# Optimization experiments

Measured on AMD Instinct MI355X. Metric: run time of the kernel, lower is better.

The kernel has to match this reference:

```python
import jax, jax.numpy as jnp
import numpy as np

WS = 7          # window size
NH = 12         # attention heads
D_STATE = 64    # mamba d_state
HEADDIM = 64    # mamba headdim


def layernorm(x, w, b):
    mu = jnp.mean(x, axis=-1, keepdims=True)
    var = jnp.mean((x - mu) ** 2, axis=-1, keepdims=True)
    return (x - mu) * jax.lax.rsqrt(var + 1e-5) * w + b


def mamba2(x, W_in, conv_w, conv_b, dt_bias, A_log, D, mnorm_w, W_out):
    # Mamba2 (SSD) forward: in_proj -> causal depthwise conv+silu -> selective scan -> gated RMSNorm -> out_proj
    B, L, dm = x.shape
    nheads = dt_bias.shape[0]
    d_inner = nheads * HEADDIM
    zxbcdt = x @ W_in                                   # (B,L,2*d_inner+2*d_state+nheads)
    z = zxbcdt[..., :d_inner]
    xBC = zxbcdt[..., d_inner:2 * d_inner + 2 * D_STATE]
    dt = zxbcdt[..., -nheads:]
    conv_dim = xBC.shape[-1]
    pad = conv_w.shape[-1] - 1
    xBC_t = jnp.swapaxes(xBC, 1, 2)                     # (B, conv_dim, L)
    conv_out = jax.lax.conv_general_dilated(
        xBC_t, conv_w[:, None, :], window_strides=(1,), padding=[(pad, 0)],
        feature_group_count=conv_dim, dimension_numbers=('NCH', 'OIH', 'NCH'))
    xBC = jax.nn.silu(jnp.swapaxes(conv_out, 1, 2) + conv_b)
    xs = xBC[..., :d_inner]
    Bm = xBC[..., d_inner:d_inner + D_STATE]            # (B,L,n)
    Cm = xBC[..., d_inner + D_STATE:]                   # (B,L,n)
    dt = jax.nn.softplus(dt + dt_bias)                  # (B,L,h)
    A = -jnp.exp(A_log)                                 # (h,)
    dA = jnp.exp(dt * A)                                # (B,L,h)
    xh = xs.reshape(B, L, nheads, HEADDIM)              # (B,L,h,p)

    def step(h, inp):
        dA_t, dt_t, x_t, B_t, C_t = inp                 # (B,h),(B,h),(B,h,p),(B,n),(B,n)
        dBx = (dt_t[..., None] * x_t)[..., None] * B_t[:, None, None, :]
        h = h * dA_t[..., None, None] + dBx             # (B,h,p,n)
        y = jnp.einsum('bhpn,bn->bhp', h, C_t)
        return h, y

    sw = lambda a: jnp.swapaxes(a, 0, 1)                # time-major
    h0 = jnp.zeros((B, nheads, HEADDIM, D_STATE), x.dtype)
    _, ys = jax.lax.scan(step, h0, (sw(dA), sw(dt), sw(xh), sw(Bm), sw(Cm)))
    y = jnp.swapaxes(ys, 0, 1) + D[None, None, :, None] * xh   # (B,L,h,p)
    y = y.reshape(B, L, d_inner)
    g = y * jax.nn.silu(z)                              # gated RMSNorm (norm_before_gate=False)
    g = g * jax.lax.rsqrt(jnp.mean(g * g, axis=-1, keepdims=True) + 1e-5) * mnorm_w
    return g @ W_out


def gated_window_attention(xw, qkv_w, qkv_b, gate_w, gate_b, proj_w, proj_b):
    B_, N, C = xw.shape
    hd = C // NH
    qkv = (xw @ qkv_w + qkv_b).reshape(B_, N, 3, NH, hd).transpose(2, 0, 3, 1, 4)
    q, k, v = qkv[0] * (hd ** -0.5), qkv[1], qkv[2]     # (B_,h,N,d)
    attn = jax.nn.softmax(jnp.einsum('bhnd,bhmd->bhnm', q, k), axis=-1)
    xa = jnp.einsum('bhnm,bhmd->bhnd', attn, v).transpose(0, 2, 1, 3)  # (B_,N,h,d)
    gate = jax.nn.sigmoid(xw @ gate_w + gate_b)[..., None]             # (B_,N,h,1)
    xa = (xa * gate).reshape(B_, N, C)
    return xa @ proj_w + proj_b


def lgs_forward(x, norm1_w, norm1_b, W_in, conv_w, conv_b, dt_bias, A_log, D, mnorm_w, W_out,
                qkv_w, qkv_b, gate_w, gate_b, proj_w, proj_b, fusion_w, fusion_b,
                norm2_w, norm2_b, fc1_w, fc1_b, fc2_w, fc2_b, H, W):
    B, L, C = x.shape
    shortcut = x
    xn = layernorm(x, norm1_w, norm1_b)
    # Branch A: Mamba2 global scan
    x_mamba = mamba2(xn, W_in, conv_w, conv_b, dt_bias, A_log, D, mnorm_w, W_out)
    # Branch B: gated window attention (shift_size=0 -> no roll, no mask)
    x2d = xn.reshape(B, H, W, C)
    xw = x2d.reshape(B, H // WS, WS, W // WS, WS, C).transpose(0, 1, 3, 2, 4, 5).reshape(-1, WS * WS, C)
    aw = gated_window_attention(xw, qkv_w, qkv_b, gate_w, gate_b, proj_w, proj_b)
    x_attn = aw.reshape(B, H // WS, W // WS, WS, WS, C).transpose(0, 1, 3, 2, 4, 5).reshape(B, L, C)
    # Fuse branches with 1x1 conv (== linear on channel dim)
    x_cat = jnp.concatenate([x_mamba, x_attn], axis=-1)   # (B,L,2C)
    x_fused = x_cat @ fusion_w + fusion_b
    x = shortcut + x_fused
    xn2 = layernorm(x, norm2_w, norm2_b)
    mlp = jax.nn.gelu(xn2 @ fc1_w + fc1_b, approximate=False) @ fc2_w + fc2_b
    return x + mlp


def setup_inputs() -> dict:
    key = jax.random.key(0)
    ks = jax.random.split(key, 16)
    B, H, W, C = 8, 56, 56, 384
    L = H * W
    d_inner, d_state, nheads_m, d_conv = 768, 64, 12, 4
    d_in_proj = 2 * d_inner + 2 * d_state + nheads_m   # 1676
    conv_dim = d_inner + 2 * d_state                   # 896
    s = 0.02
    return {
        'x': jax.random.normal(ks[0], (B, L, C), jnp.float32),
        'norm1_w': jnp.ones((C,), jnp.float32),
        'norm1_b': jnp.zeros((C,), jnp.float32),
        'W_in': jax.random.normal(ks[1], (C, d_in_proj), jnp.float32) * s,
        'conv_w': jax.random.normal(ks[2], (conv_dim, d_conv), jnp.float32) * 0.1,
        'conv_b': jnp.zeros((conv_dim,), jnp.float32),
        'dt_bias': jax.random.normal(ks[3], (nheads_m,), jnp.float32) * 0.5,
        'A_log': jnp.log(jax.random.uniform(ks[4], (nheads_m,), jnp.float32, 1.0, 16.0)),
        'D': jnp.ones((nheads_m,), jnp.float32),
        'mnorm_w': jnp.ones((d_inner,), jnp.float32),
        'W_out': jax.random.normal(ks[5], (d_inner, C), jnp.float32) * s,
        'qkv_w': jax.random.normal(ks[6], (C, 3 * C), jnp.float32) * s,
        'qkv_b': jnp.zeros((3 * C,), jnp.float32),
        'gate_w': jax.random.normal(ks[7], (C, NH), jnp.float32) * s,
        'gate_b': jnp.zeros((NH,), jnp.float32),
        'proj_w': jax.random.normal(ks[8], (C, C), jnp.float32) * s,
        'proj_b': jnp.zeros((C,), jnp.float32),
        'fusion_w': jax.random.normal(ks[9], (2 * C, C), jnp.float32) * s,
        'fusion_b': jnp.zeros((C,), jnp.float32),
        'norm2_w': jnp.ones((C,), jnp.float32),
        'norm2_b': jnp.zeros((C,), jnp.float32),
        'fc1_w': jax.random.normal(ks[10], (C, 4 * C), jnp.float32) * s,
        'fc1_b': jnp.zeros((4 * C,), jnp.float32),
        'fc2_w': jax.random.normal(ks[11], (4 * C, C), jnp.float32) * s,
        'fc2_b': jnp.zeros((C,), jnp.float32),
        'H': H,
        'W': W,
    }


def reference(x, norm1_w, norm1_b, W_in, conv_w, conv_b, dt_bias, A_log, D, mnorm_w, W_out,
              qkv_w, qkv_b, gate_w, gate_b, proj_w, proj_b, fusion_w, fusion_b,
              norm2_w, norm2_b, fc1_w, fc1_b, fc2_w, fc2_b, H, W):
    return lgs_forward(x, norm1_w, norm1_b, W_in, conv_w, conv_b, dt_bias, A_log, D, mnorm_w, W_out,
                       qkv_w, qkv_b, gate_w, gate_b, proj_w, proj_b, fusion_w, fusion_b,
                       norm2_w, norm2_b, fc1_w, fc1_b, fc2_w, fc2_b, H, W)
```

## Files before the change

kernel.cpp:

```cpp
#include <hip/hip_runtime.h>
#include <math.h>

static constexpr int L_SEQ  = 3136;
static constexpr int NBATCH = 8;
static constexpr int CDIM   = 384;
static constexpr int DIN    = 768;
static constexpr int NHM    = 12;
static constexpr int HDM    = 64;
static constexpr int DPROJ  = 1676;
static constexpr int CONVD  = 896;
static constexpr int NROWS  = NBATCH * L_SEQ;
static constexpr int NHA    = 12;
static constexpr int NCH    = 49;
static constexpr int CHT    = 64;
static constexpr int CTK    = 28;
static constexpr int ZXLD   = 1024;

typedef __attribute__((ext_vector_type(8))) short short8;
typedef __attribute__((ext_vector_type(8))) unsigned short ushort8;
typedef __attribute__((ext_vector_type(4))) float f32x4;
typedef const unsigned int __attribute__((address_space(1)))* gua_t;
typedef unsigned int __attribute__((address_space(3)))* lua_t;

__device__ __forceinline__ float siluf(float x) { return x / (1.f + __expf(-x)); }
__device__ __forceinline__ unsigned short f2bf(float f) {
  unsigned int u = __float_as_uint(f);
  u += 0x7fff + ((u >> 16) & 1);
  return (unsigned short)(u >> 16);
}
__device__ __forceinline__ float bf2f(unsigned short h) {
  return __uint_as_float(((unsigned int)h) << 16);
}
__device__ __forceinline__ float fast_erff(float x) {
  float ax = fabsf(x);
  float tt = 1.f / (1.f + 0.3275911f * ax);
  float y = tt * (0.254829592f + tt * (-0.284496736f + tt * (1.421413741f +
            tt * (-1.453152027f + tt * 1.061405429f))));
  float r = 1.f - y * __expf(-ax * ax);
  return copysignf(r, x);
}

__global__ __launch_bounds__(256) void ln_kernel(const float* __restrict__ in,
    const float* __restrict__ w, const float* __restrict__ b, unsigned short* __restrict__ out) {
  int wave = threadIdx.x >> 6, lane = threadIdx.x & 63;
  int row = blockIdx.x * 4 + wave;
  if (row >= NROWS) return;
  const float* r = in + (size_t)row * CDIM;
  float2 v[3];
  float s1 = 0.f, s2 = 0.f;
#pragma unroll
  for (int q = 0; q < 3; q++) {
    v[q] = *(const float2*)&r[q * 128 + lane * 2];
    s1 += v[q].x + v[q].y;
    s2 += v[q].x * v[q].x + v[q].y * v[q].y;
  }
#pragma unroll
  for (int o = 32; o > 0; o >>= 1) { s1 += __shfl_xor(s1, o, 64); s2 += __shfl_xor(s2, o, 64); }
  float mu = s1 * (1.f / 384.f);
  float var = s2 * (1.f / 384.f) - mu * mu;
  float rs = rsqrtf(var + 1e-5f);
  unsigned short* o = out + (size_t)row * CDIM;
#pragma unroll
  for (int q = 0; q < 3; q++) {
    int c = q * 128 + lane * 2;
    float2 wv = *(const float2*)&w[c];
    float2 bv = *(const float2*)&b[c];
    float ox = (v[q].x - mu) * rs * wv.x + bv.x;
    float oy = (v[q].y - mu) * rs * wv.y + bv.y;
    unsigned int pk = (unsigned int)f2bf(ox) | ((unsigned int)f2bf(oy) << 16);
    *(unsigned int*)&o[c] = pk;
  }
}

__global__ __launch_bounds__(256) void wconv_kernel(const float* __restrict__ W,
    unsigned short* __restrict__ WT, int K, int N, int ldw) {
  __shared__ float tile[32][33];
  int k0 = blockIdx.x * 32, n0 = blockIdx.y * 32;
  int tx = threadIdx.x & 31, ty = threadIdx.x >> 5;
#pragma unroll
  for (int j = 0; j < 4; j++) {
    int k = k0 + ty + j * 8;
    int n = n0 + tx;
    tile[ty + j * 8][tx] = (n < N) ? W[(size_t)k * ldw + n] : 0.f;
  }
  __syncthreads();
#pragma unroll
  for (int j = 0; j < 4; j++) {
    int n = n0 + ty + j * 8;
    int k = k0 + tx;
    WT[(size_t)n * K + k] = f2bf(tile[tx][ty + j * 8]);
  }
}

template<int ACT, bool HASBIAS, bool HASRES, bool OUTBF>
__global__ __launch_bounds__(256, 4) void gemm_bf(
    const unsigned short* __restrict__ A, const unsigned short* __restrict__ WT,
    void* __restrict__ Cp, const float* __restrict__ bias,
    const float* __restrict__ res, int ldr,
    int M, int N, int K, int lda, int ldc, int coff)
{
  __shared__ unsigned short SMEM[16384];
  int t = threadIdx.x;
  int gx = gridDim.x;
  int nwg = gx * gridDim.y;
  int orig = blockIdx.y * gx + blockIdx.x;
  int qq = nwg >> 3, rr = nwg & 7;
  int xcd = orig & 7, seq = orig >> 3;
  int wgid = (xcd < rr ? xcd * (qq + 1) : rr * (qq + 1) + (xcd - rr) * qq) + seq;
  int m0 = (wgid / gx) * 128, n0 = (wgid % gx) * 128;

  int lane = t & 63, w = t >> 6;
  int wr = (w >> 1) * 64, wc = (w & 1) * 64;
  int fl = lane & 15, kq = lane >> 4;
  int so = (kq ^ ((lane >> 1) & 3)) * 8;

  int srow = t >> 2, sq = t & 3;
  int q0 = sq ^ ((srow >> 1) & 3);
  const unsigned short* pA0 = A  + (size_t)(m0 + srow) * lda + q0 * 8;
  const unsigned short* pA1 = A  + (size_t)(m0 + 64 + srow) * lda + q0 * 8;
  const unsigned short* pW0 = WT + (size_t)(n0 + srow) * K + q0 * 8;
  const unsigned short* pW1 = WT + (size_t)(n0 + 64 + srow) * K + q0 * 8;

  f32x4 acc[4][4];
#pragma unroll
  for (int i = 0; i < 4; i++)
#pragma unroll
    for (int j = 0; j < 4; j++) acc[i][j] = (f32x4)0.f;

  auto STAGE = [&](int buf) {
    unsigned short* as = SMEM + buf * 4096;
    unsigned short* ws = SMEM + 8192 + buf * 4096;
    __builtin_amdgcn_global_load_lds((gua_t)pA0, (lua_t)as + t * 4, 16, 0, 0);
    __builtin_amdgcn_global_load_lds((gua_t)pA1, (lua_t)(as + 2048) + t * 4, 16, 0, 0);
    __builtin_amdgcn_global_load_lds((gua_t)pW0, (lua_t)ws + t * 4, 16, 0, 0);
    __builtin_amdgcn_global_load_lds((gua_t)pW1, (lua_t)(ws + 2048) + t * 4, 16, 0, 0);
    pA0 += 32; pA1 += 32; pW0 += 32; pW1 += 32;
  };

  int nk = K >> 5;
  STAGE(0);
  asm volatile("s_waitcnt vmcnt(0)" ::: "memory");
  __builtin_amdgcn_s_barrier();
  asm volatile("" ::: "memory");
  __builtin_amdgcn_sched_barrier(0);
  int buf = 0;
  for (int ks = 0; ks < nk; ks++) {
    if (ks + 1 < nk) STAGE(buf ^ 1);
    const unsigned short* as = SMEM + buf * 4096;
    const unsigned short* ws = SMEM + 8192 + buf * 4096;
    short8 af[4], bfr[4];
#pragma unroll
    for (int mi = 0; mi < 4; mi++) af[mi] = *(const short8*)&as[(wr + mi * 16 + fl) * 32 + so];
#pragma unroll
    for (int ni = 0; ni < 4; ni++) bfr[ni] = *(const short8*)&ws[(wc + ni * 16 + fl) * 32 + so];
#pragma unroll
    for (int mi = 0; mi < 4; mi++)
#pragma unroll
      for (int ni = 0; ni < 4; ni++)
        acc[mi][ni] = __builtin_amdgcn_mfma_f32_16x16x32_bf16(af[mi], bfr[ni], acc[mi][ni], 0, 0, 0);
    if (ks + 1 < nk) {
      asm volatile("s_waitcnt vmcnt(0)" ::: "memory");
      __builtin_amdgcn_s_barrier();
      asm volatile("" ::: "memory");
      __builtin_amdgcn_sched_barrier(0);
      buf ^= 1;
    }
  }
  int rbase = kq * 4, cl = fl;
  if (OUTBF) {
    __builtin_amdgcn_s_barrier();
#pragma unroll
    for (int mi = 0; mi < 4; mi++)
#pragma unroll
      for (int ni = 0; ni < 4; ni++) {
        int n = wc + ni * 16 + cl;
        float bv = HASBIAS ? bias[n0 + n] : 0.f;
#pragma unroll
        for (int r = 0; r < 4; r++) {
          float v = acc[mi][ni][r] + bv;
          if (ACT == 1) v = 0.5f * v * (1.f + fast_erff(v * 0.70710678118654752f));
          SMEM[(wr + mi * 16 + rbase + r) * 128 + n] = f2bf(v);
        }
      }
    __builtin_amdgcn_s_barrier();
    unsigned short* outp = (unsigned short*)Cp + coff + n0;
#pragma unroll
    for (int it2 = 0; it2 < 8; it2++) {
      int c = it2 * 256 + t;
      int rrow = c >> 4, c8 = (c & 15) * 8;
      ushort8 v8 = *(const ushort8*)&SMEM[rrow * 128 + c8];
      *(ushort8*)&outp[(size_t)(m0 + rrow) * ldc + c8] = v8;
    }
  } else {
#pragma unroll
    for (int mi = 0; mi < 4; mi++) {
#pragma unroll
      for (int ni = 0; ni < 4; ni++) {
        int n = n0 + wc + ni * 16 + cl;
        if (n >= N) continue;
#pragma unroll
        for (int r = 0; r < 4; r++) {
          int m = m0 + wr + mi * 16 + rbase + r;
          float v = acc[mi][ni][r];
          if (HASBIAS) v += bias[n];
          if (ACT == 1) v = 0.5f * v * (1.f + fast_erff(v * 0.70710678118654752f));
          if (HASRES) v += res[(size_t)m * ldr + n];
          ((float*)Cp)[(size_t)m * ldc + coff + n] = v;
        }
      }
    }
  }
}

__global__ void dtprep_kernel(const unsigned short* __restrict__ ZX, const float* __restrict__ dt_bias,
    const float* __restrict__ A_log, float* __restrict__ DT, float* __restrict__ DA) {
  int idx = blockIdx.x * blockDim.x + threadIdx.x;
  if (idx >= NROWS * NHM) return;
  int h = idx % NHM;
  int row = idx / NHM;
  float v = bf2f(ZX[(size_t)row * ZXLD + 896 + h]) + dt_bias[h];
  float sp = (v > 20.f) ? v : log1pf(expf(v));
  DT[idx] = sp;
  DA[idx] = -expf(A_log[h]) * sp;
}

__global__ __launch_bounds__(256) void conv_bf_kernel(const unsigned short* __restrict__ xbc,
    const float* __restrict__ cw, const float* __restrict__ cb, unsigned short* __restrict__ XC,
    int ldin) {
  int t = blockIdx.x * 256 + threadIdx.x;
  int c8 = t % 112;
  int rg = t / 112;
  int b = rg / 112, lc = rg % 112;
  int l0 = lc * CTK;
  int c0 = c8 * 8;
  float w0[8], w1[8], w2[8], w3[8], bq[8];
#pragma unroll
  for (int i = 0; i < 8; i++) {
    bq[i] = cb[c0 + i];
    float4 w4 = *(const float4*)&cw[(c0 + i) * 4];
    w0[i] = w4.x; w1[i] = w4.y; w2[i] = w4.z; w3[i] = w4.w;
  }
  const unsigned short* base = xbc + (size_t)b * L_SEQ * ldin + c0;
  unsigned short* obase = XC + (size_t)b * L_SEQ * CONVD + c0;
  ushort8 h0 = (ushort8)0, h1 = (ushort8)0, h2 = (ushort8)0;
  if (l0 >= 3) {
    h0 = *(const ushort8*)&base[(size_t)(l0 - 3) * ldin];
    h1 = *(const ushort8*)&base[(size_t)(l0 - 2) * ldin];
    h2 = *(const ushort8*)&base[(size_t)(l0 - 1) * ldin];
  }
  for (int i = 0; i < CTK; i++) {
    ushort8 cur = *(const ushort8*)&base[(size_t)(l0 + i) * ldin];
    ushort8 ov;
#pragma unroll
    for (int q = 0; q < 8; q++) {
      float acc = bq[q] + w0[q] * bf2f(h0[q]) + w1[q] * bf2f(h1[q])
                + w2[q] * bf2f(h2[q]) + w3[q] * bf2f(cur[q]);
      ov[q] = f2bf(siluf(acc));
    }
    *(ushort8*)&obase[(size_t)(l0 + i) * CONVD] = ov;
    h0 = h1; h1 = h2; h2 = cur;
  }
}

__global__ __launch_bounds__(256) void mscan1_kernel(const unsigned short* __restrict__ XC,
    const float* __restrict__ dtp, const float* __restrict__ dta,
    float* __restrict__ H, float* __restrict__ QS) {
  __shared__ unsigned short Xt[64 * 72];
  __shared__ unsigned short Bt[64 * 72];
  __shared__ float lcs[64];
  __shared__ float wss[64];
  int ch = blockIdx.x, bh = blockIdx.y;
  int b = bh / NHM, head = bh - b * NHM;
  int t = threadIdx.x;
  int l0 = ch * CHT;
  const unsigned short* xcb = XC + ((size_t)b * L_SEQ + l0) * CONVD;
  if (t < 64) {
    size_t ro = ((size_t)b * L_SEQ + l0 + t) * NHM + head;
    float s = dta[ro];
#pragma unroll
    for (int o = 1; o < 64; o <<= 1) {
      float u = __shfl_up(s, o, 64);
      if (t >= o) s += u;
    }
    float lc63 = __shfl(s, 63, 64);
    lcs[t] = s;
    wss[t] = dtp[ro] * __expf(lc63 - s);
    if (t == 63) QS[bh * NCH + ch] = __expf(s);
  }
  __syncthreads();
#pragma unroll
  for (int it = 0; it < 16; it++) {
    int e = it * 256 + t;
    int j = e >> 6, cc = e & 63;
    const unsigned short* rowp = xcb + (size_t)j * CONVD;
    Xt[cc * 72 + j] = rowp[head * HDM + cc];
    Bt[cc * 72 + j] = f2bf(bf2f(rowp[768 + cc]) * wss[j]);
  }
  __syncthreads();
  int lane = t & 63, w = t >> 6;
  int wr = (w >> 1) * 32, wc = (w & 1) * 32;
  int fl = lane & 15, kq = lane >> 4;
  f32x4 acc[2][2];
#pragma unroll
  for (int i = 0; i < 2; i++)
#pragma unroll
    for (int j = 0; j < 2; j++) acc[i][j] = (f32x4)0.f;
#pragma unroll
  for (int kk = 0; kk < 2; kk++) {
    short8 af[2], bfr[2];
#pragma unroll
    for (int mi = 0; mi < 2; mi++)
      af[mi] = *(const short8*)&Xt[(wr + mi * 16 + fl) * 72 + kk * 32 + kq * 8];
#pragma unroll
    for (int ni = 0; ni < 2; ni++)
      bfr[ni] = *(const short8*)&Bt[(wc + ni * 16 + fl) * 72 + kk * 32 + kq * 8];
#pragma unroll
    for (int mi = 0; mi < 2; mi++)
#pragma unroll
      for (int ni = 0; ni < 2; ni++)
        acc[mi][ni] = __builtin_amdgcn_mfma_f32_16x16x32_bf16(af[mi], bfr[ni], acc[mi][ni], 0, 0, 0);
  }
  float* Hp = H + ((size_t)bh * NCH + ch) * 4096;
  int rbase = kq * 4, cl = fl;
#pragma unroll
  for (int mi = 0; mi < 2; mi++)
#pragma unroll
    for (int ni = 0; ni < 2; ni++)
#pragma unroll
      for (int r = 0; r < 4; r++)
        Hp[(size_t)(wr + mi * 16 + rbase + r) * 64 + wc + ni * 16 + cl] = acc[mi][ni][r];
}

__global__ __launch_bounds__(64) void scomb_kernel(float* __restrict__ H,
    const float* __restrict__ QS) {
  int bh = blockIdx.x;
  int e = (blockIdx.y * 64 + threadIdx.x) * 4;
  float4 cur = make_float4(0.f, 0.f, 0.f, 0.f);
  for (int s = 0; s < NCH; s++) {
    float* Hp = H + ((size_t)bh * NCH + s) * 4096 + e;
    float q = QS[bh * NCH + s];
    float4 tmp = *(float4*)Hp;
    *(float4*)Hp = cur;
    cur.x = q * cur.x + tmp.x;
    cur.y = q * cur.y + tmp.y;
    cur.z = q * cur.z + tmp.z;
    cur.w = q * cur.w + tmp.w;
  }
}

__global__ __launch_bounds__(256) void mscan2_kernel(const unsigned short* __restrict__ XC,
    const float* __restrict__ dtp, const float* __restrict__ dta,
    const float* __restrict__ H, const float* __restrict__ Dp,
    unsigned short* __restrict__ Ybf) {
  __shared__ unsigned short Cs[64 * 72];
  __shared__ unsigned short Bs[64 * 72];
  __shared__ unsigned short Xt[64 * 72];
  __shared__ unsigned short Hs[64 * 72];
  __shared__ unsigned short Ss[64 * 72];
  __shared__ float lcs[64];
  __shared__ float dts[64];
  int ch = blockIdx.x, bh = blockIdx.y;
  int b = bh / NHM, head = bh - b * NHM;
  int t = threadIdx.x;
  int l0 = ch * CHT;
  const unsigned short* xcb = XC + ((size_t)b * L_SEQ + l0) * CONVD;
  const float* Hg = H + ((size_t)bh * NCH + ch) * 4096;
  if (t < 64) {
    size_t ro = ((size_t)b * L_SEQ + l0 + t) * NHM + head;
    float s = dta[ro];
#pragma unroll
    for (int o = 1; o < 64; o <<= 1) {
      float u = __shfl_up(s, o, 64);
      if (t >= o) s += u;
    }
    lcs[t] = s;
    dts[t] = dtp[ro];
  }
#pragma unroll
  for (int it = 0; it < 16; it++) {
    int e = it * 256 + t;
    int j = e >> 6, cc = e & 63;
    const unsigned short* rowp = xcb + (size_t)j * CONVD;
    Xt[cc * 72 + j] = rowp[head * HDM + cc];
    Bs[j * 72 + cc] = rowp[768 + cc];
    Cs[j * 72 + cc] = rowp[832 + cc];
    Hs[j * 72 + cc] = f2bf(Hg[e]);
  }
  __syncthreads();
  int lane = t & 63, w = t >> 6;
  int wr = (w >> 1) * 32, wc = (w & 1) * 32;
  int fl = lane & 15, kq = lane >> 4;
  int rbase = kq * 4, cl = fl;
  f32x4 sacc[2][2];
#pragma unroll
  for (int i = 0; i < 2; i++)
#pragma unroll
    for (int j = 0; j < 2; j++) sacc[i][j] = (f32x4)0.f;
#pragma unroll
  for (int kk = 0; kk < 2; kk++) {
    short8 af[2], bfr[2];
#pragma unroll
    for (int mi = 0; mi < 2; mi++)
      af[mi] = *(const short8*)&Cs[(wr + mi * 16 + fl) * 72 + kk * 32 + kq * 8];
#pragma unroll
    for (int ni = 0; ni < 2; ni++)
      bfr[ni] = *(const short8*)&Bs[(wc + ni * 16 + fl) * 72 + kk * 32 + kq * 8];
#pragma unroll
    for (int mi = 0; mi < 2; mi++)
#pragma unroll
      for (int ni = 0; ni < 2; ni++)
        sacc[mi][ni] = __builtin_amdgcn_mfma_f32_16x16x32_bf16(af[mi], bfr[ni], sacc[mi][ni], 0, 0, 0);
  }
  __syncthreads();
#pragma unroll
  for (int mi = 0; mi < 2; mi++)
#pragma unroll
    for (int ni = 0; ni < 2; ni++)
#pragma unroll
      for (int r = 0; r < 4; r++) {
        int i = wr + mi * 16 + rbase + r;
        int j = wc + ni * 16 + cl;
        float v = (j <= i) ? sacc[mi][ni][r] * dts[j] * __expf(lcs[i] - lcs[j]) : 0.f;
        Ss[i * 72 + j] = f2bf(v);
      }
#pragma unroll
  for (int it = 0; it < 16; it++) {
    int e = it * 256 + t;
    int i = e >> 6, n = e & 63;
    float cv = bf2f(Cs[i * 72 + n]) * __expf(lcs[i]);
    Cs[i * 72 + n] = f2bf(cv);
  }
  __syncthreads();
  f32x4 yacc[2][2];
#pragma unroll
  for (int i = 0; i < 2; i++)
#pragma unroll
    for (int j = 0; j < 2; j++) yacc[i][j] = (f32x4)0.f;
#pragma unroll
  for (int kk = 0; kk < 2; kk++) {
    short8 af[2], bfr[2];
#pragma unroll
    for (int mi = 0; mi < 2; mi++)
      af[mi] = *(const short8*)&Ss[(wr + mi * 16 + fl) * 72 + kk * 32 + kq * 8];
#pragma unroll
    for (int ni = 0; ni < 2; ni++)
      bfr[ni] = *(const short8*)&Xt[(wc + ni * 16 + fl) * 72 + kk * 32 + kq * 8];
#pragma unroll
    for (int mi = 0; mi < 2; mi++)
#pragma unroll
      for (int ni = 0; ni < 2; ni++)
        yacc[mi][ni] = __builtin_amdgcn_mfma_f32_16x16x32_bf16(af[mi], bfr[ni], yacc[mi][ni], 0, 0, 0);
  }
#pragma unroll
  for (int kk = 0; kk < 2; kk++) {
    short8 af[2], bfr[2];
#pragma unroll
    for (int mi = 0; mi < 2; mi++)
      af[mi] = *(const short8*)&Cs[(wr + mi * 16 + fl) * 72 + kk * 32 + kq * 8];
#pragma unroll
    for (int ni = 0; ni < 2; ni++)
      bfr[ni] = *(const short8*)&Hs[(wc + ni * 16 + fl) * 72 + kk * 32 + kq * 8];
#pragma unroll
    for (int mi = 0; mi < 2; mi++)
#pragma unroll
      for (int ni = 0; ni < 2; ni++)
        yacc[mi][ni] = __builtin_amdgcn_mfma_f32_16x16x32_bf16(af[mi], bfr[ni], yacc[mi][ni], 0, 0, 0);
  }
  float Dh = Dp[head];
  unsigned short* yb = Ybf + ((size_t)b * L_SEQ + l0) * DIN + head * HDM;
#pragma unroll
  for (int mi = 0; mi < 2; mi++)
#pragma unroll
    for (int ni = 0; ni < 2; ni++)
#pragma unroll
      for (int r = 0; r < 4; r++) {
        int i = wr + mi * 16 + rbase + r;
        int p = wc + ni * 16 + cl;
        float xval = bf2f(Xt[p * 72 + i]);
        yb[(size_t)i * DIN + p] = f2bf(yacc[mi][ni][r] + Dh * xval);
      }
}

__global__ __launch_bounds__(256) void gate_rms_kernel(unsigned short* __restrict__ Y,
    const unsigned short* __restrict__ Z, const float* __restrict__ mw) {
  int wave = threadIdx.x >> 6, lane = threadIdx.x & 63;
  int row = blockIdx.x * 4 + wave;
  if (row >= NROWS) return;
  unsigned short* y = Y + (size_t)row * DIN;
  const unsigned short* z = Z + (size_t)row * DIN;
  float g[12];
  float ss = 0.f;
#pragma unroll
  for (int q = 0; q < 3; q++) {
    int c = q * 256 + lane * 4;
    uint2 yu = *(const uint2*)&y[c];
    uint2 zu = *(const uint2*)&z[c];
    float y0 = bf2f((unsigned short)(yu.x & 0xffff));
    float y1 = bf2f((unsigned short)(yu.x >> 16));
    float y2 = bf2f((unsigned short)(yu.y & 0xffff));
    float y3 = bf2f((unsigned short)(yu.y >> 16));
    float z0 = bf2f((unsigned short)(zu.x & 0xffff));
    float z1 = bf2f((unsigned short)(zu.x >> 16));
    float z2 = bf2f((unsigned short)(zu.y & 0xffff));
    float z3 = bf2f((unsigned short)(zu.y >> 16));
    float g0 = y0 * siluf(z0), g1 = y1 * siluf(z1);
    float g2 = y2 * siluf(z2), g3 = y3 * siluf(z3);
    ss += g0 * g0 + g1 * g1 + g2 * g2 + g3 * g3;
    g[q * 4 + 0] = g0; g[q * 4 + 1] = g1; g[q * 4 + 2] = g2; g[q * 4 + 3] = g3;
  }
#pragma unroll
  for (int o = 32; o > 0; o >>= 1) ss += __shfl_xor(ss, o, 64);
  float rs = rsqrtf(ss * (1.f / 768.f) + 1e-5f);
#pragma unroll
  for (int q = 0; q < 3; q++) {
    int c = q * 256 + lane * 4;
    float4 m = *(const float4*)&mw[c];
    unsigned int lo = (unsigned int)f2bf(g[q*4+0] * rs * m.x) | ((unsigned int)f2bf(g[q*4+1] * rs * m.y) << 16);
    unsigned int hi = (unsigned int)f2bf(g[q*4+2] * rs * m.z) | ((unsigned int)f2bf(g[q*4+3] * rs * m.w) << 16);
    uint2 pk; pk.x = lo; pk.y = hi;
    *(uint2*)&y[c] = pk;
  }
}

__global__ __launch_bounds__(256) void attgate_kernel(const unsigned short* __restrict__ XN,
    const float* __restrict__ gw, const float* __restrict__ gb, float* __restrict__ G) {
  int wave = threadIdx.x >> 6, lane = threadIdx.x & 63;
  int row = blockIdx.x * 4 + wave;
  if (row >= NROWS) return;
  const unsigned short* x = XN + (size_t)row * CDIM;
  float acc[12] = {};
#pragma unroll
  for (int q = 0; q < 6; q++) {
    int k = q * 64 + lane;
    float xv = bf2f(x[k]);
    const float* wr = gw + (size_t)k * 12;
    float4 w0 = *(const float4*)&wr[0];
    float4 w1 = *(const float4*)&wr[4];
    float4 w2 = *(const float4*)&wr[8];
    acc[0] += xv * w0.x; acc[1] += xv * w0.y; acc[2]  += xv * w0.z; acc[3]  += xv * w0.w;
    acc[4] += xv * w1.x; acc[5] += xv * w1.y; acc[6]  += xv * w1.z; acc[7]  += xv * w1.w;
    acc[8] += xv * w2.x; acc[9] += xv * w2.y; acc[10] += xv * w2.z; acc[11] += xv * w2.w;
  }
#pragma unroll
  for (int h = 0; h < 12; h++)
#pragma unroll
    for (int o = 32; o > 0; o >>= 1) acc[h] += __shfl_xor(acc[h], o, 64);
  if (lane == 0) {
#pragma unroll
    for (int h = 0; h < 12; h++) {
      float v = acc[h] + gb[h];
      G[(size_t)row * 12 + h] = 1.f / (1.f + expf(-v));
    }
  }
}

__global__ __launch_bounds__(64) void attn_kernel(const unsigned short* __restrict__ QKV,
    const float* __restrict__ G, unsigned short* __restrict__ XA) {
  __shared__ unsigned short Pl[64 * 72];
  __shared__ unsigned short Vt[32 * 72];
  int blk = blockIdx.x;
  int head = blk % NHA;
  int win = blk / NHA;
  int b = win >> 6;
  int wrw = win & 63;
  int wy = wrw >> 3, wx = wrw & 7;
  int lane = threadIdx.x;
  int fl = lane & 15, kq = lane >> 4;
  const float scale = 0.17677669529663688f;
  size_t bbase = (size_t)b * L_SEQ;
  const unsigned short* qb = QKV + head * 32;

  short8 aq[4], bk[4];
#pragma unroll
  for (int ti = 0; ti < 4; ti++) {
    int tok = ti * 16 + fl; if (tok > 48) tok = 48;
    int iy = tok / 7, ix = tok - iy * 7;
    size_t r = bbase + (size_t)(wy * 7 + iy) * 56 + wx * 7 + ix;
    aq[ti] = *(const short8*)&qb[r * 1152 + kq * 8];
    bk[ti] = *(const short8*)&qb[r * 1152 + 384 + kq * 8];
  }
#pragma unroll
  for (int it = 0; it < 4; it++) {
    int j = (lane >> 2) + it * 16;
    int dc = (lane & 3) * 8;
    ushort8 v8 = (ushort8)0;
    if (j <= 48) {
      int iy = j / 7, ix = j - iy * 7;
      size_t r = bbase + (size_t)(wy * 7 + iy) * 56 + wx * 7 + ix;
      v8 = *(const ushort8*)&qb[r * 1152 + 768 + dc];
    }
#pragma unroll
    for (int q2 = 0; q2 < 8; q2++) {
      int d = dc + q2;
      Vt[d * 72 + (((j >> 3) ^ (d >> 3)) << 3) + (j & 7)] = v8[q2];
    }
  }
  f32x4 sacc[4][4];
#pragma unroll
  for (int tj = 0; tj < 4; tj++)
#pragma unroll
    for (int ti = 0; ti < 4; ti++)
      sacc[tj][ti] = __builtin_amdgcn_mfma_f32_16x16x32_bf16(bk[tj], aq[ti], (f32x4)0.f, 0, 0, 0);
#pragma unroll
  for (int ti = 0; ti < 4; ti++) {
    float mx = -1e30f;
#pragma unroll
    for (int tj = 0; tj < 4; tj++)
#pragma unroll
      for (int r = 0; r < 4; r++) {
        int j = tj * 16 + kq * 4 + r;
        float v = (j < 49) ? sacc[tj][ti][r] * scale : -1e30f;
        sacc[tj][ti][r] = v;
        mx = fmaxf(mx, v);
      }
    mx = fmaxf(mx, __shfl_xor(mx, 16, 64));
    mx = fmaxf(mx, __shfl_xor(mx, 32, 64));
    float sum = 0.f;
#pragma unroll
    for (int tj = 0; tj < 4; tj++)
#pragma unroll
      for (int r = 0; r < 4; r++) {
        float e = __expf(sacc[tj][ti][r] - mx);
        sacc[tj][ti][r] = e;
        sum += e;
      }
    sum += __shfl_xor(sum, 16, 64);
    sum += __shfl_xor(sum, 32, 64);
    float inv = 1.f / sum;
    int i = ti * 16 + fl;
#pragma unroll
    for (int tj = 0; tj < 4; tj++)
#pragma unroll
      for (int r = 0; r < 4; r++) {
        int j = tj * 16 + kq * 4 + r;
        Pl[i * 72 + j] = f2bf(sacc[tj][ti][r] * inv);
      }
  }
  f32x4 oacc[4][2];
#pragma unroll
  for (int i2 = 0; i2 < 4; i2++)
#pragma unroll
    for (int nd = 0; nd < 2; nd++) oacc[i2][nd] = (f32x4)0.f;
#pragma unroll
  for (int kk = 0; kk < 2; kk++) {
    short8 ap[4], bv[2];
#pragma unroll
    for (int i2 = 0; i2 < 4; i2++)
      ap[i2] = *(const short8*)&Pl[(i2 * 16 + fl) * 72 + kk * 32 + kq * 8];
#pragma unroll
    for (int nd = 0; nd < 2; nd++) {
      int d = nd * 16 + fl;
      bv[nd] = *(const short8*)&Vt[d * 72 + (((kk * 4 + kq) ^ (d >> 3)) << 3)];
    }
#pragma unroll
    for (int i2 = 0; i2 < 4; i2++)
#pragma unroll
      for (int nd = 0; nd < 2; nd++)
        oacc[i2][nd] = __builtin_amdgcn_mfma_f32_16x16x32_bf16(ap[i2], bv[nd], oacc[i2][nd], 0, 0, 0);
  }
#pragma unroll
  for (int i2 = 0; i2 < 4; i2++) {
#pragma unroll
    for (int r = 0; r < 4; r++) {
      int i = i2 * 16 + kq * 4 + r;
      if (i > 48) continue;
      int iy = i / 7, ix = i - iy * 7;
      size_t rg = bbase + (size_t)(wy * 7 + iy) * 56 + wx * 7 + ix;
      float g = G[rg * 12 + head];
#pragma unroll
      for (int nd = 0; nd < 2; nd++)
        XA[rg * CDIM + head * 32 + nd * 16 + fl] = f2bf(oacc[i2][nd][r] * g);
    }
  }
}

extern "C" void kernel_launch(void* const* d_in, const int* in_sizes, int n_in,
                              void* d_out, int out_size, void* d_ws, size_t ws_size,
                              hipStream_t stream) {
  const float* x        = (const float*)d_in[0];
  const float* norm1_w  = (const float*)d_in[1];
  const float* norm1_b  = (const float*)d_in[2];
  const float* W_in     = (const float*)d_in[3];
  const float* conv_w   = (const float*)d_in[4];
  const float* conv_b   = (const float*)d_in[5];
  const float* dt_bias  = (const float*)d_in[6];
  const float* A_log    = (const float*)d_in[7];
  const float* Dp       = (const float*)d_in[8];
  const float* mnorm_w  = (const float*)d_in[9];
  const float* W_out    = (const float*)d_in[10];
  const float* qkv_w    = (const float*)d_in[11];
  const float* qkv_b    = (const float*)d_in[12];
  const float* gate_w   = (const float*)d_in[13];
  const float* gate_b   = (const float*)d_in[14];
  const float* proj_w   = (const float*)d_in[15];
  const float* proj_b   = (const float*)d_in[16];
  const float* fusion_w = (const float*)d_in[17];
  const float* fusion_b = (const float*)d_in[18];
  const float* norm2_w  = (const float*)d_in[19];
  const float* norm2_b  = (const float*)d_in[20];
  const float* fc1_w    = (const float*)d_in[21];
  const float* fc1_b    = (const float*)d_in[22];
  const float* fc2_w    = (const float*)d_in[23];
  const float* fc2_b    = (const float*)d_in[24];
  float* OUT = (float*)d_out;

  float* ws = (float*)d_ws;
  unsigned short* XNBF = (unsigned short*)ws;
  float* XC_  = ws + 4816896;
  float* SCR  = XC_ + 22478848;
  unsigned short* YBF = (unsigned short*)(SCR + 22478848);
  unsigned short* WT  = (unsigned short*)(SCR + 22478848 + 9633792);
  float* DT_ = (float*)(WT + 3047424);
  float* DA_ = DT_ + 301056;
  float* G_  = DA_ + 301056;
  float* QS_ = G_  + 301056;

  unsigned short* ZXBF  = (unsigned short*)SCR;
  unsigned short* XCBF  = (unsigned short*)XC_;
  float* H_ = SCR;
  unsigned short* ZBF   = (unsigned short*)SCR;
  unsigned short* QKVBF = (unsigned short*)SCR;
  unsigned short* M1BF  = (unsigned short*)SCR;
  unsigned short* CATBF = (unsigned short*)XC_;
  unsigned short* XABF  = (unsigned short*)(XC_ + 9633792);

  unsigned short* wt_xbcdt = WT;
  unsigned short* wt_z    = WT + 393216;
  unsigned short* wt_out  = WT + 688128;
  unsigned short* wt_qkv  = WT + 983040;
  unsigned short* wt_proj = WT + 1425408;
  unsigned short* wt_fus  = WT + 1572864;
  unsigned short* wt_fc1  = WT + 1867776;
  unsigned short* wt_fc2  = WT + 2457600;

  wconv_kernel<<<dim3(12,  29), 256, 0, stream>>>(W_in + 768,  wt_xbcdt, 384, 908, DPROJ);
  wconv_kernel<<<dim3(12,  24), 256, 0, stream>>>(W_in,        wt_z,    384,  768, DPROJ);
  wconv_kernel<<<dim3(24,  12), 256, 0, stream>>>(W_out,       wt_out,  768,  384, 384);
  wconv_kernel<<<dim3(12,  36), 256, 0, stream>>>(qkv_w,       wt_qkv,  384, 1152, 1152);
  wconv_kernel<<<dim3(12,  12), 256, 0, stream>>>(proj_w,      wt_proj, 384,  384, 384);
  wconv_kernel<<<dim3(24,  12), 256, 0, stream>>>(fusion_w,    wt_fus,  768,  384, 384);
  wconv_kernel<<<dim3(12,  48), 256, 0, stream>>>(fc1_w,       wt_fc1,  384, 1536, 1536);
  wconv_kernel<<<dim3(48,  12), 256, 0, stream>>>(fc2_w,       wt_fc2, 1536,  384, 384);

  ln_kernel<<<6272, 256, 0, stream>>>(x, norm1_w, norm1_b, XNBF);

  gemm_bf<0, false, false, true><<<dim3(8, 196), 256, 0, stream>>>(
      XNBF, wt_xbcdt, ZXBF, nullptr, nullptr, 0, NROWS, 908, CDIM, CDIM, ZXLD, 0);
  conv_bf_kernel<<<392, 256, 0, stream>>>(ZXBF, conv_w, conv_b, XCBF, ZXLD);
  dtprep_kernel<<<(NROWS * NHM + 255) / 256, 256, 0, stream>>>(ZXBF, dt_bias, A_log, DT_, DA_);

  mscan1_kernel<<<dim3(NCH, 96), 256, 0, stream>>>(XCBF, DT_, DA_, H_, QS_);
  scomb_kernel<<<dim3(96, 16), 64, 0, stream>>>(H_, QS_);
  mscan2_kernel<<<dim3(NCH, 96), 256, 0, stream>>>(XCBF, DT_, DA_, H_, Dp, YBF);

  gemm_bf<0, false, false, true><<<dim3(6, 196), 256, 0, stream>>>(
      XNBF, wt_z, ZBF, nullptr, nullptr, 0, NROWS, DIN, CDIM, CDIM, DIN, 0);
  gate_rms_kernel<<<6272, 256, 0, stream>>>(YBF, ZBF, mnorm_w);

  gemm_bf<0, false, false, true><<<dim3(3, 196), 256, 0, stream>>>(
      YBF, wt_out, CATBF, nullptr, nullptr, 0, NROWS, CDIM, DIN, DIN, 2 * CDIM, 0);

  attgate_kernel<<<6272, 256, 0, stream>>>(XNBF, gate_w, gate_b, G_);

  gemm_bf<0, true, false, true><<<dim3(9, 196), 256, 0, stream>>>(
      XNBF, wt_qkv, QKVBF, qkv_b, nullptr, 0, NROWS, 3 * CDIM, CDIM, CDIM, 3 * CDIM, 0);
  attn_kernel<<<512 * NHA, 64, 0, stream>>>(QKVBF, G_, XABF);

  gemm_bf<0, true, false, true><<<dim3(3, 196), 256, 0, stream>>>(
      XABF, wt_proj, CATBF, proj_b, nullptr, 0, NROWS, CDIM, CDIM, CDIM, 2 * CDIM, CDIM);

  gemm_bf<0, true, true, false><<<dim3(3, 196), 256, 0, stream>>>(
      CATBF, wt_fus, OUT, fusion_b, x, CDIM, NROWS, CDIM, 2 * CDIM, 2 * CDIM, CDIM, 0);

  ln_kernel<<<6272, 256, 0, stream>>>(OUT, norm2_w, norm2_b, XNBF);

  gemm_bf<1, true, false, true><<<dim3(12, 196), 256, 0, stream>>>(
      XNBF, wt_fc1, M1BF, fc1_b, nullptr, 0, NROWS, 4 * CDIM, CDIM, CDIM, 4 * CDIM, 0);
  gemm_bf<0, true, true, false><<<dim3(3, 196), 256, 0, stream>>>(
      M1BF, wt_fc2, OUT, fc2_b, OUT, CDIM, NROWS, CDIM, 4 * CDIM, 4 * CDIM, CDIM, 0);
}
```

Before: 656.0 us.

## Transpose MFMA operands for row-contiguous epilogue stores, add cheaper GELU and bf16 packing

```diff
diff --git a/kernel.cpp b/kernel.cpp
--- a/kernel.cpp
+++ b/kernel.cpp
@@ -31,13 +31,19 @@
 __device__ __forceinline__ float bf2f(unsigned short h) {
   return __uint_as_float(((unsigned int)h) << 16);
 }
-__device__ __forceinline__ float fast_erff(float x) {
-  float ax = fabsf(x);
-  float tt = 1.f / (1.f + 0.3275911f * ax);
-  float y = tt * (0.254829592f + tt * (-0.284496736f + tt * (1.421413741f +
-            tt * (-1.453152027f + tt * 1.061405429f))));
-  float r = 1.f - y * __expf(-ax * ax);
-  return copysignf(r, x);
+__device__ __forceinline__ float geluf(float v) {
+  float ax = fabsf(v) * 0.70710678118654752f;
+  float t = __builtin_amdgcn_rcpf(fmaf(0.47047f, ax, 1.f));
+  float p = t * fmaf(t, fmaf(t, 0.7478556f, -0.0958798f), 0.3480242f);
+  float e = __expf(-ax * ax);
+  float r = 1.f - p * e;
+  float h = 0.5f * v;
+  return fmaf(fabsf(h), r, h);
+}
+__device__ __forceinline__ unsigned int pk_bf16(float lo, float hi) {
+  unsigned int d;
+  asm("v_cvt_pk_bf16_f32 %0, %1, %2" : "=v"(d) : "v"(lo), "v"(hi));
+  return d;
 }
 
 __global__ __launch_bounds__(256) void ln_kernel(const float* __restrict__ in,
@@ -67,8 +73,7 @@
     float2 bv = *(const float2*)&b[c];
     float ox = (v[q].x - mu) * rs * wv.x + bv.x;
     float oy = (v[q].y - mu) * rs * wv.y + bv.y;
-    unsigned int pk = (unsigned int)f2bf(ox) | ((unsigned int)f2bf(oy) << 16);
-    *(unsigned int*)&o[c] = pk;
+    *(unsigned int*)&o[c] = pk_bf16(ox, oy);
   }
 }
 
@@ -157,7 +162,7 @@
     for (int mi = 0; mi < 4; mi++)
 #pragma unroll
       for (int ni = 0; ni < 4; ni++)
-        acc[mi][ni] = __builtin_amdgcn_mfma_f32_16x16x32_bf16(af[mi], bfr[ni], acc[mi][ni], 0, 0, 0);
+        acc[mi][ni] = __builtin_amdgcn_mfma_f32_16x16x32_bf16(bfr[ni], af[mi], acc[mi][ni], 0, 0, 0);
     if (ks + 1 < nk) {
       asm volatile("s_waitcnt vmcnt(0)" ::: "memory");
       __builtin_amdgcn_s_barrier();
@@ -166,47 +171,49 @@
       buf ^= 1;
     }
   }
-  int rbase = kq * 4, cl = fl;
+  int rbase = kq * 4;
   if (OUTBF) {
-    __builtin_amdgcn_s_barrier();
-#pragma unroll
-    for (int mi = 0; mi < 4; mi++)
+    unsigned short* outp = (unsigned short*)Cp + coff;
+#pragma unroll
+    for (int mi = 0; mi < 4; mi++) {
+      int m = m0 + wr + mi * 16 + fl;
+      unsigned short* rowp = outp + (size_t)m * ldc + n0;
 #pragma unroll
       for (int ni = 0; ni < 4; ni++) {
-        int n = wc + ni * 16 + cl;
-        float bv = HASBIAS ? bias[n0 + n] : 0.f;
-#pragma unroll
-        for (int r = 0; r < 4; r++) {
-          float v = acc[mi][ni][r] + bv;
-          if (ACT == 1) v = 0.5f * v * (1.f + fast_erff(v * 0.70710678118654752f));
-          SMEM[(wr + mi * 16 + rbase + r) * 128 + n] = f2bf(v);
+        int nb = wc + ni * 16 + rbase;
+        float v0 = acc[mi][ni][0], v1 = acc[mi][ni][1];
+        float v2 = acc[mi][ni][2], v3 = acc[mi][ni][3];
+        if (HASBIAS) {
+          float4 bv = *(const float4*)&bias[n0 + nb];
+          v0 += bv.x; v1 += bv.y; v2 += bv.z; v3 += bv.w;
         }
+        if (ACT == 1) { v0 = geluf(v0); v1 = geluf(v1); v2 = geluf(v2); v3 = geluf(v3); }
+        uint2 pk; pk.x = pk_bf16(v0, v1); pk.y = pk_bf16(v2, v3);
+        *(uint2*)&rowp[nb] = pk;
       }
-    __builtin_amdgcn_s_barrier();
-    unsigned short* outp = (unsigned short*)Cp + coff + n0;
-#pragma unroll
-    for (int it2 = 0; it2 < 8; it2++) {
-      int c = it2 * 256 + t;
-      int rrow = c >> 4, c8 = (c & 15) * 8;
-      ushort8 v8 = *(const ushort8*)&SMEM[rrow * 128 + c8];
-      *(ushort8*)&outp[(size_t)(m0 + rrow) * ldc + c8] = v8;
     }
   } else {
+    float* outp = (float*)Cp + coff;
 #pragma unroll
     for (int mi = 0; mi < 4; mi++) {
+      int m = m0 + wr + mi * 16 + fl;
+      float* rowp = outp + (size_t)m * ldc + n0;
 #pragma unroll
       for (int ni = 0; ni < 4; ni++) {
-        int n = n0 + wc + ni * 16 + cl;
-        if (n >= N) continue;
-#pragma unroll
-        for (int r = 0; r < 4; r++) {
-          int m = m0 + wr + mi * 16 + rbase + r;
-          float v = acc[mi][ni][r];
-          if (HASBIAS) v += bias[n];
-          if (ACT == 1) v = 0.5f * v * (1.f + fast_erff(v * 0.70710678118654752f));
-          if (HASRES) v += res[(size_t)m * ldr + n];
-          ((float*)Cp)[(size_t)m * ldc + coff + n] = v;
+        int nb = wc + ni * 16 + rbase;
+        float4 v;
+        v.x = acc[mi][ni][0]; v.y = acc[mi][ni][1];
+        v.z = acc[mi][ni][2]; v.w = acc[mi][ni][3];
+        if (HASBIAS) {
+          float4 bv = *(const float4*)&bias[n0 + nb];
+          v.x += bv.x; v.y += bv.y; v.z += bv.z; v.w += bv.w;
         }
+        if (ACT == 1) { v.x = geluf(v.x); v.y = geluf(v.y); v.z = geluf(v.z); v.w = geluf(v.w); }
+        if (HASRES) {
+          float4 rv = *(const float4*)&res[(size_t)m * ldr + n0 + nb];
+          v.x += rv.x; v.y += rv.y; v.z += rv.z; v.w += rv.w;
+        }
+        *(float4*)&rowp[nb] = v;
       }
     }
   }
@@ -515,9 +522,9 @@
   for (int q = 0; q < 3; q++) {
     int c = q * 256 + lane * 4;
     float4 m = *(const float4*)&mw[c];
-    unsigned int lo = (unsigned int)f2bf(g[q*4+0] * rs * m.x) | ((unsigned int)f2bf(g[q*4+1] * rs * m.y) << 16);
-    unsigned int hi = (unsigned int)f2bf(g[q*4+2] * rs * m.z) | ((unsigned int)f2bf(g[q*4+3] * rs * m.w) << 16);
-    uint2 pk; pk.x = lo; pk.y = hi;
+    uint2 pk;
+    pk.x = pk_bf16(g[q*4+0] * rs * m.x, g[q*4+1] * rs * m.y);
+    pk.y = pk_bf16(g[q*4+2] * rs * m.z, g[q*4+3] * rs * m.w);
     *(uint2*)&y[c] = pk;
   }
 }
```

New measurement: 664.7 us. Within noise of the previous version (+1.3%).
